# Kernel tuning notes

Hardware: AMD Instinct MI355X
Metric: run time of the kernel (lower is better)

## Reference

```python
import jax, jax.numpy as jnp
import numpy as np

N_NODES = 100000
N_EDGES = 1600000
D_IN = 128
HIDDEN = 64
N_CLASSES = 10
N_GRAPHS = 512


def setup_inputs() -> dict:
    key = jax.random.key(0)
    ks = jax.random.split(key, 9)
    x = jax.random.normal(ks[0], (N_NODES, D_IN), dtype=jnp.float32)
    edge_index = jax.random.randint(ks[1], (2, N_EDGES), 0, N_NODES, dtype=jnp.int32)
    batch = jnp.sort(jax.random.randint(ks[2], (N_NODES,), 0, N_GRAPHS, dtype=jnp.int32))
    # GCNConv: lin (no bias) + separate bias added after aggregation
    s1 = 1.0 / np.sqrt(D_IN)
    s2 = 1.0 / np.sqrt(HIDDEN)
    W1 = jax.random.uniform(ks[3], (D_IN, HIDDEN), jnp.float32, -s1, s1)
    b1 = jnp.zeros((HIDDEN,), jnp.float32)
    W2 = jax.random.uniform(ks[4], (HIDDEN, HIDDEN), jnp.float32, -s2, s2)
    b2 = jnp.zeros((HIDDEN,), jnp.float32)
    Wfc = jax.random.uniform(ks[5], (HIDDEN, N_CLASSES), jnp.float32, -s2, s2)
    bfc = jax.random.uniform(ks[6], (N_CLASSES,), jnp.float32, -s2, s2)
    return {"x": x, "edge_index": edge_index, "batch": batch,
            "W1": W1, "b1": b1, "W2": W2, "b2": b2, "Wfc": Wfc, "bfc": bfc}


def gcn_conv(x, src, dst, W, b, n_nodes):
    # symmetric normalization with added self-loops (PyG gcn_norm defaults)
    deg = jnp.zeros((n_nodes,), x.dtype).at[dst].add(1.0) + 1.0  # +1 self-loop
    dinv = jax.lax.rsqrt(deg)
    h = x @ W  # [N, out]
    coef = (dinv[src] * dinv[dst])[:, None]          # [E, 1]
    msg = h[src] * coef                               # [E, out]
    agg = jax.ops.segment_sum(msg, dst, num_segments=n_nodes)
    agg = agg + h * (dinv * dinv)[:, None]            # self-loop contribution
    return agg + b


def reference(x, edge_index, batch, W1, b1, W2, b2, Wfc, bfc):
    src, dst = edge_index[0], edge_index[1]
    n_nodes = x.shape[0]
    h = gcn_conv(x, src, dst, W1, b1, n_nodes)
    h = jax.nn.relu(h)
    # dropout skipped (inference, training=False)
    h = gcn_conv(h, src, dst, W2, b2, n_nodes)
    h = jax.nn.relu(h)
    # global mean pool over graphs
    sums = jax.ops.segment_sum(h, batch, num_segments=N_GRAPHS)
    cnts = jax.ops.segment_sum(jnp.ones((n_nodes,), h.dtype), batch, num_segments=N_GRAPHS)
    pooled = sums / jnp.maximum(cnts, 1.0)[:, None]   # [G, hidden]
    logits = pooled @ Wfc + bfc                        # [G, classes]
    return jax.nn.log_softmax(logits, axis=1)
```

## Files before the change

### kernel.cpp

```cpp
#include <hip/hip_runtime.h>
#include <cstdint>
#include <cstddef>

#define N_NODES   100000
#define N_EDGES   1600000
#define D_IN      128
#define HIDDEN    64
#define N_GRAPHS  512
#define N_CLASSES 10

#define NB   196
#define EB   1563
#define EB4  391
#define NBE  (NB * EB)
#define BCAP 12288
#define PSLOTS 8

typedef __attribute__((ext_vector_type(8))) short bf16x8;
typedef __attribute__((ext_vector_type(4))) float f32x4;
typedef __attribute__((ext_vector_type(2))) float f32x2;

__device__ inline float bf2f(unsigned short u) {
    return __uint_as_float(((unsigned int)u) << 16);
}
__device__ inline unsigned short f2bf(float f) {
    unsigned int x = __float_as_uint(f);
    return (unsigned short)((x + 0x7FFF + ((x >> 16) & 1)) >> 16);
}

__global__ __launch_bounds__(256)
void scan1_kernel(const int* __restrict__ in, int* __restrict__ bsum, int n) {
    __shared__ int lds[256];
    int tid = threadIdx.x;
    int base = blockIdx.x * 4096 + tid * 16;
    int s = 0;
#pragma unroll
    for (int j = 0; j < 16; j++) { int i = base + j; if (i < n) s += in[i]; }
    lds[tid] = s; __syncthreads();
    for (int off = 128; off > 0; off >>= 1) {
        if (tid < off) lds[tid] += lds[tid + off];
        __syncthreads();
    }
    if (tid == 0) bsum[blockIdx.x] = lds[0];
}

__global__ __launch_bounds__(256)
void scan2_kernel(int* __restrict__ bsum, int* __restrict__ out, int nb, int n) {
    __shared__ int lds[256];
    int tid = threadIdx.x;
    int v = (tid < nb) ? bsum[tid] : 0;
    lds[tid] = v; __syncthreads();
    for (int off = 1; off < 256; off <<= 1) {
        int t = (tid >= off) ? lds[tid - off] : 0;
        __syncthreads();
        lds[tid] += t;
        __syncthreads();
    }
    if (tid < nb) bsum[tid] = lds[tid] - v;
    if (tid == 255) out[n] = lds[255];
}

__global__ __launch_bounds__(256)
void scan3_kernel(const int* __restrict__ in, const int* __restrict__ bsum,
                  int* __restrict__ out, int n) {
    __shared__ int lds[256];
    int tid = threadIdx.x;
    int base = blockIdx.x * 4096 + tid * 16;
    int v[16]; int s = 0;
#pragma unroll
    for (int j = 0; j < 16; j++) {
        int i = base + j;
        v[j] = (i < n) ? in[i] : 0;
        s += v[j];
    }
    lds[tid] = s; __syncthreads();
    for (int off = 1; off < 256; off <<= 1) {
        int t = (tid >= off) ? lds[tid - off] : 0;
        __syncthreads();
        lds[tid] += t;
        __syncthreads();
    }
    int ex = lds[tid] - s + bsum[blockIdx.x];
#pragma unroll
    for (int j = 0; j < 16; j++) {
        int i = base + j;
        if (i < n) { out[i] = ex; ex += v[j]; }
    }
}

__global__ __launch_bounds__(256)
void hist_kernel(const int* __restrict__ dst, int* __restrict__ HA) {
    __shared__ int cnt[NB];
    const int tid = threadIdx.x;
    const int hb = blockIdx.x;
    for (int i = tid; i < NB; i += 256) cnt[i] = 0;
    __syncthreads();
    int base = hb * 1024 + tid;
#pragma unroll
    for (int j = 0; j < 4; j++) {
        int t = base + j * 256;
        if (t < N_EDGES) atomicAdd(&cnt[dst[t] >> 9], 1);
    }
    __syncthreads();
    for (int b = tid; b < NB; b += 256) HA[b * EB + hb] = cnt[b];
}

__global__ __launch_bounds__(256)
void scatterA2_kernel(const int* __restrict__ src, const int* __restrict__ dst,
                      const int* __restrict__ posA, unsigned int* __restrict__ edgeA) {
    __shared__ int off[NB];
    int tid = threadIdx.x, blk = blockIdx.x;
    for (int b = tid; b < NB; b += 256) off[b] = posA[b * EB + blk * 4];
    __syncthreads();
    int base = blk * 4096 + tid;
#pragma unroll
    for (int j = 0; j < 16; j++) {
        int t = base + j * 256;
        if (t < N_EDGES) {
            int d = dst[t];
            unsigned int pk = (((unsigned int)(d & 511)) << 17) | (unsigned int)src[t];
            int r = atomicAdd(&off[d >> 9], 1);
            edgeA[r] = pk;
        }
    }
}

__global__ __launch_bounds__(256)
void passB_kernel(const int* __restrict__ posA, const unsigned int* __restrict__ edgeA,
                  int* __restrict__ noffs, float* __restrict__ dinv,
                  int* __restrict__ srcs2) {
    __shared__ int hist[512];
    __shared__ int off[512];
    __shared__ int ps[256];
    __shared__ int srcs_l[BCAP];

    int tid = threadIdx.x, b = blockIdx.x;
    int e0 = posA[b * EB];
    int e1 = posA[(b + 1) * EB];
    int n0 = b << 9;
    int nn = min(512, N_NODES - n0);
    int len = e1 - e0;

    hist[tid] = 0; hist[tid + 256] = 0;
    __syncthreads();
    for (int i = e0 + tid; i < e1; i += 256) atomicAdd(&hist[edgeA[i] >> 17], 1);
    __syncthreads();

    for (int n = tid; n < nn; n += 256) dinv[n0 + n] = rsqrtf((float)hist[n] + 1.0f);

    int a0 = hist[2 * tid], a1 = hist[2 * tid + 1];
    ps[tid] = a0 + a1;
    __syncthreads();
    for (int d = 1; d < 256; d <<= 1) {
        int v = (tid >= d) ? ps[tid - d] : 0;
        __syncthreads();
        ps[tid] += v;
        __syncthreads();
    }
    int pre = ps[tid] - (a0 + a1);
    off[2 * tid] = pre;
    off[2 * tid + 1] = pre + a0;
    __syncthreads();

    for (int n = tid; n < nn; n += 256) noffs[n0 + n] = e0 + off[n];
    if (b == NB - 1 && tid == 0) noffs[N_NODES] = N_EDGES;
    __syncthreads();

    if (len <= BCAP) {
        for (int i = e0 + tid; i < e1; i += 256) {
            unsigned int e = edgeA[i];
            int r = atomicAdd(&off[e >> 17], 1);
            srcs_l[r] = (int)(e & 0x1FFFFu);
        }
        __syncthreads();
        for (int i = tid; i < len; i += 256) srcs2[e0 + i] = srcs_l[i];
    } else {
        for (int i = e0 + tid; i < e1; i += 256) {
            unsigned int e = edgeA[i];
            int r = atomicAdd(&off[e >> 17], 1);
            srcs2[e0 + r] = (int)(e & 0x1FFFFu);
        }
    }
}

__global__ __launch_bounds__(512)
void gemm1_kernel(const float* __restrict__ X, const float* __restrict__ W,
                  const float* __restrict__ dinv, unsigned short* __restrict__ H,
                  int n_rows) {
    constexpr int K  = D_IN;
    constexpr int KP = K + 8;
    __shared__ unsigned short Wt[64 * KP];

    const int tid  = threadIdx.x;
    const int row0 = blockIdx.x * 128;

    for (int i = tid; i < K * 64; i += 512) {
        int k = i >> 6;
        int n = i & 63;
        Wt[n * KP + k] = f2bf(W[i]);
    }

    const int wave = tid >> 6;
    const int lane = tid & 63;
    const int lrow = lane & 15;
    const int quad = lane >> 4;
    const int m = wave * 16 + lrow;
    const int row = row0 + m;
    const bool valid = row < n_rows;

    float4 xa[8];
    if (valid) {
        const float4* xr4 = (const float4*)(X + (size_t)row * K);
#pragma unroll
        for (int kt = 0; kt < 4; kt++) {
            int q = (kt * 32 + quad * 8) >> 2;
            xa[2 * kt]     = xr4[q];
            xa[2 * kt + 1] = xr4[q + 1];
        }
    } else {
#pragma unroll
        for (int j = 0; j < 8; j++) xa[j] = make_float4(0.f, 0.f, 0.f, 0.f);
    }
    __syncthreads();

    f32x4 acc0 = {0.f, 0.f, 0.f, 0.f};
    f32x4 acc1 = {0.f, 0.f, 0.f, 0.f};
    f32x4 acc2 = {0.f, 0.f, 0.f, 0.f};
    f32x4 acc3 = {0.f, 0.f, 0.f, 0.f};

#pragma unroll
    for (int kt = 0; kt < 4; kt++) {
        int k0 = kt * 32 + quad * 8;
        const float* f = (const float*)&xa[2 * kt];
        bf16x8 a;
#pragma unroll
        for (int j = 0; j < 8; j++) a[j] = (short)f2bf(f[j]);
        bf16x8 b0 = *(const bf16x8*)&Wt[(0 * 16 + lrow) * KP + k0];
        bf16x8 b1 = *(const bf16x8*)&Wt[(1 * 16 + lrow) * KP + k0];
        bf16x8 b2 = *(const bf16x8*)&Wt[(2 * 16 + lrow) * KP + k0];
        bf16x8 b3 = *(const bf16x8*)&Wt[(3 * 16 + lrow) * KP + k0];
        acc0 = __builtin_amdgcn_mfma_f32_16x16x32_bf16(a, b0, acc0, 0, 0, 0);
        acc1 = __builtin_amdgcn_mfma_f32_16x16x32_bf16(a, b1, acc1, 0, 0, 0);
        acc2 = __builtin_amdgcn_mfma_f32_16x16x32_bf16(a, b2, acc2, 0, 0, 0);
        acc3 = __builtin_amdgcn_mfma_f32_16x16x32_bf16(a, b3, acc3, 0, 0, 0);
    }

    f32x4 accs[4] = {acc0, acc1, acc2, acc3};
#pragma unroll
    for (int r = 0; r < 4; r++) {
        int orow = row0 + wave * 16 + quad * 4 + r;
        if (orow < n_rows) {
            float dv = dinv[orow];
#pragma unroll
            for (int c = 0; c < 4; c++)
                H[(size_t)orow * 64 + c * 16 + lrow] = f2bf(accs[c][r] * dv);
        }
    }
}

__device__ inline void upk_add(int4 u, float* acc) {
    unsigned int a = (unsigned int)u.x, b = (unsigned int)u.y;
    unsigned int d = (unsigned int)u.z, e = (unsigned int)u.w;
    acc[0] += __uint_as_float(a << 16);
    acc[1] += __uint_as_float(a & 0xFFFF0000u);
    acc[2] += __uint_as_float(b << 16);
    acc[3] += __uint_as_float(b & 0xFFFF0000u);
    acc[4] += __uint_as_float(d << 16);
    acc[5] += __uint_as_float(d & 0xFFFF0000u);
    acc[6] += __uint_as_float(e << 16);
    acc[7] += __uint_as_float(e & 0xFFFF0000u);
}

__device__ inline void upk8_add(int2 u, float* acc) {
    f32x2 p0 = __builtin_amdgcn_cvt_pk_f32_fp8(u.x, false);
    f32x2 p1 = __builtin_amdgcn_cvt_pk_f32_fp8(u.x, true);
    f32x2 p2 = __builtin_amdgcn_cvt_pk_f32_fp8(u.y, false);
    f32x2 p3 = __builtin_amdgcn_cvt_pk_f32_fp8(u.y, true);
    acc[0] += p0.x; acc[1] += p0.y;
    acc[2] += p1.x; acc[3] += p1.y;
    acc[4] += p2.x; acc[5] += p2.y;
    acc[6] += p3.x; acc[7] += p3.y;
}

__global__ __launch_bounds__(512)
void gather1_gemm2_kernel(const int* __restrict__ offs, const int* __restrict__ srcs,
                          const float* __restrict__ dinv, const unsigned short* __restrict__ h,
                          const float* __restrict__ b1v, const float* __restrict__ W2,
                          unsigned char* __restrict__ H8, int n_nodes) {
    constexpr int KP = 72;
    __shared__ unsigned short Hs[64 * KP];
    __shared__ unsigned short Wt[64 * KP];

    const int tid   = threadIdx.x;
    const int node0 = blockIdx.x * 64;

    for (int i = tid; i < 64 * 64; i += 512) {
        int k = i >> 6;
        int n = i & 63;
        Wt[n * KP + k] = f2bf(W2[i]);
    }

    const int g    = tid >> 3;
    const int node = node0 + g;
    const int cg   = (tid & 7) * 8;

    float acc[8];
#pragma unroll
    for (int j = 0; j < 8; j++) acc[j] = 0.f;
    float dn = 0.f;

    if (node < n_nodes) {
        dn = dinv[node];
        int4 us = *(const int4*)(h + (size_t)node * 64 + cg);
        upk_add(us, acc);

        int i = offs[node];
        const int i1 = offs[node + 1];
        int rem = i1 - i;
        if (rem > 0) {
            int s[8];
#pragma unroll
            for (int j = 0; j < 8; j++) s[j] = srcs[i + (j < rem ? j : rem - 1)];
            while (rem > 0) {
                int4 u8[8];
#pragma unroll
                for (int j = 0; j < 8; j++)
                    u8[j] = *(const int4*)(h + (size_t)s[j] * 64 + cg);
                const int cur  = rem < 8 ? rem : 8;
                const int ni   = i + cur;
                const int nrem = rem - cur;
                if (nrem > 0) {
#pragma unroll
                    for (int j = 0; j < 8; j++)
                        s[j] = srcs[ni + (j < nrem ? j : nrem - 1)];
                }
#pragma unroll
                for (int j = 0; j < 8; j++) { if (j < cur) upk_add(u8[j], acc); }
                i = ni; rem = nrem;
            }
        }
    }

    {
        float4 bv0 = *(const float4*)(b1v + cg);
        float4 bv1 = *(const float4*)(b1v + cg + 4);
        float r0 = fmaxf(dn * acc[0] + bv0.x, 0.f);
        float r1 = fmaxf(dn * acc[1] + bv0.y, 0.f);
        float r2 = fmaxf(dn * acc[2] + bv0.z, 0.f);
        float r3 = fmaxf(dn * acc[3] + bv0.w, 0.f);
        float r4 = fmaxf(dn * acc[4] + bv1.x, 0.f);
        float r5 = fmaxf(dn * acc[5] + bv1.y, 0.f);
        float r6 = fmaxf(dn * acc[6] + bv1.z, 0.f);
        float r7 = fmaxf(dn * acc[7] + bv1.w, 0.f);
        ushort4 p0 = make_ushort4(f2bf(r0), f2bf(r1), f2bf(r2), f2bf(r3));
        ushort4 p1 = make_ushort4(f2bf(r4), f2bf(r5), f2bf(r6), f2bf(r7));
        *(ushort4*)&Hs[g * KP + cg]     = p0;
        *(ushort4*)&Hs[g * KP + cg + 4] = p1;
    }
    __syncthreads();

    const int wave = tid >> 6;
    const int lane = tid & 63;
    const int lrow = lane & 15;
    const int quad = lane >> 4;
    const int rt = (wave & 3) * 16;
    const int ct = (wave >> 2) * 32;
    const int m = rt + lrow;

    f32x4 acc0 = {0.f, 0.f, 0.f, 0.f};
    f32x4 acc1 = {0.f, 0.f, 0.f, 0.f};
#pragma unroll
    for (int kt = 0; kt < 2; kt++) {
        int k0 = kt * 32 + quad * 8;
        bf16x8 a  = *(const bf16x8*)&Hs[m * KP + k0];
        bf16x8 w0 = *(const bf16x8*)&Wt[(ct + lrow) * KP + k0];
        bf16x8 w1 = *(const bf16x8*)&Wt[(ct + 16 + lrow) * KP + k0];
        acc0 = __builtin_amdgcn_mfma_f32_16x16x32_bf16(a, w0, acc0, 0, 0, 0);
        acc1 = __builtin_amdgcn_mfma_f32_16x16x32_bf16(a, w1, acc1, 0, 0, 0);
    }

    f32x4 accs[2] = {acc0, acc1};
#pragma unroll
    for (int r = 0; r < 4; r++) {
        int row = node0 + rt + quad * 4 + r;
        if (row < n_nodes) {
            float dv = dinv[row];
#pragma unroll
            for (int c = 0; c < 2; c++) {
                float v = accs[c][r] * dv;
                int p = __builtin_amdgcn_cvt_pk_fp8_f32(v, v, 0, false);
                H8[(size_t)row * 64 + ct + c * 16 + lrow] = (unsigned char)(p & 0xFF);
            }
        }
    }
}

__global__ __launch_bounds__(256)
void gather_fp8_pool_kernel(const int* __restrict__ offs, const int* __restrict__ srcs,
                            const float* __restrict__ dinv, const unsigned char* __restrict__ h8,
                            const float* __restrict__ b, const int* __restrict__ batch,
                            float* __restrict__ pooled, float* __restrict__ cnt,
                            int n_nodes) {
    __shared__ float pacc[PSLOTS][64];
    __shared__ float lcnt[PSLOTS];
    __shared__ int sg[2];

    int tid = threadIdx.x;
    int node0 = blockIdx.x * 32;
    int lastn = min(node0 + 31, n_nodes - 1);
    for (int i = tid; i < PSLOTS * 64; i += 256) ((float*)pacc)[i] = 0.f;
    if (tid < PSLOTS) lcnt[tid] = 0.f;
    if (tid == 0) { sg[0] = batch[min(node0, n_nodes - 1)]; sg[1] = batch[lastn]; }
    __syncthreads();
    int g0 = sg[0];
    bool single = (sg[0] == sg[1]);

    int node = node0 + (tid >> 3);
    int cg = (tid & 7) * 8;

    float r[8];
#pragma unroll
    for (int j = 0; j < 8; j++) r[j] = 0.f;

    if (node < n_nodes) {
        float dn = dinv[node];
        float acc[8];
#pragma unroll
        for (int j = 0; j < 8; j++) acc[j] = 0.f;
        {
            int2 u = *(const int2*)(h8 + (size_t)node * 64 + cg);
            upk8_add(u, acc);
        }

        int i = offs[node];
        const int i1 = offs[node + 1];
        int rem = i1 - i;
        if (rem > 0) {
            int s[8];
#pragma unroll
            for (int j = 0; j < 8; j++) s[j] = srcs[i + (j < rem ? j : rem - 1)];
            while (rem > 0) {
                int2 u8[8];
#pragma unroll
                for (int j = 0; j < 8; j++)
                    u8[j] = *(const int2*)(h8 + (size_t)s[j] * 64 + cg);
                const int cur  = rem < 8 ? rem : 8;
                const int ni   = i + cur;
                const int nrem = rem - cur;
                if (nrem > 0) {
#pragma unroll
                    for (int j = 0; j < 8; j++)
                        s[j] = srcs[ni + (j < nrem ? j : nrem - 1)];
                }
#pragma unroll
                for (int j = 0; j < 8; j++) { if (j < cur) upk8_add(u8[j], acc); }
                i = ni; rem = nrem;
            }
        }

        float4 b0 = *(const float4*)(b + cg);
        float4 b1 = *(const float4*)(b + cg + 4);
        r[0] = fmaxf(dn * acc[0] + b0.x, 0.f);
        r[1] = fmaxf(dn * acc[1] + b0.y, 0.f);
        r[2] = fmaxf(dn * acc[2] + b0.z, 0.f);
        r[3] = fmaxf(dn * acc[3] + b0.w, 0.f);
        r[4] = fmaxf(dn * acc[4] + b1.x, 0.f);
        r[5] = fmaxf(dn * acc[5] + b1.y, 0.f);
        r[6] = fmaxf(dn * acc[6] + b1.z, 0.f);
        r[7] = fmaxf(dn * acc[7] + b1.w, 0.f);
    }

    if (single) {
#pragma unroll
        for (int j = 0; j < 8; j++) {
            float v = r[j];
            v += __shfl_xor(v, 8);
            v += __shfl_xor(v, 16);
            v += __shfl_xor(v, 32);
            r[j] = v;
        }
        int wave = tid >> 6;
        int lane = tid & 63;
        if (lane < 8) {
#pragma unroll
            for (int j = 0; j < 8; j++) pacc[wave][lane * 8 + j] = r[j];
        }
        __syncthreads();
        if (tid < 64) {
            float s = pacc[0][tid] + pacc[1][tid] + pacc[2][tid] + pacc[3][tid];
            if (s != 0.f) unsafeAtomicAdd(&pooled[(size_t)g0 * 64 + tid], s);
        }
        if (tid == 0) {
            int valid = min(32, n_nodes - node0);
            unsafeAtomicAdd(&cnt[g0], (float)valid);
        }
    } else {
        if (node < n_nodes) {
            int g = batch[node];
            int slot = g - g0;
            if (slot < PSLOTS) {
#pragma unroll
                for (int j = 0; j < 8; j++) atomicAdd(&pacc[slot][cg + j], r[j]);
                if ((tid & 7) == 0) atomicAdd(&lcnt[slot], 1.f);
            } else {
#pragma unroll
                for (int j = 0; j < 8; j++) unsafeAtomicAdd(&pooled[(size_t)g * 64 + cg + j], r[j]);
                if ((tid & 7) == 0) unsafeAtomicAdd(&cnt[g], 1.f);
            }
        }
        __syncthreads();
        for (int i = tid; i < PSLOTS * 64; i += 256) {
            float v = ((float*)pacc)[i];
            if (v != 0.f) unsafeAtomicAdd(&pooled[(size_t)(g0 + (i >> 6)) * 64 + (i & 63)], v);
        }
        if (tid < PSLOTS && lcnt[tid] != 0.f) unsafeAtomicAdd(&cnt[g0 + tid], lcnt[tid]);
    }
}

__global__ __launch_bounds__(256)
void head_kernel(const float* __restrict__ pooled, const float* __restrict__ cnt,
                 const float* __restrict__ Wfc, const float* __restrict__ bfc,
                 float* __restrict__ out) {
    __shared__ float Ws[HIDDEN * N_CLASSES];
    __shared__ float bs[N_CLASSES];
    int tid = threadIdx.x;
    for (int i = tid; i < HIDDEN * N_CLASSES; i += 256) Ws[i] = Wfc[i];
    if (tid < N_CLASSES) bs[tid] = bfc[tid];
    __syncthreads();

    int g = blockIdx.x * 256 + tid;
    if (g >= N_GRAPHS) return;

    float inv = 1.f / fmaxf(cnt[g], 1.f);
    float p[HIDDEN];
#pragma unroll
    for (int k = 0; k < HIDDEN; k++) p[k] = pooled[(size_t)g * 64 + k] * inv;

    float lg[N_CLASSES];
    float m = -1e30f;
#pragma unroll
    for (int j = 0; j < N_CLASSES; j++) {
        float a = bs[j];
#pragma unroll
        for (int k = 0; k < HIDDEN; k++) a += p[k] * Ws[k * N_CLASSES + j];
        lg[j] = a;
        m = fmaxf(m, a);
    }
    float s = 0.f;
#pragma unroll
    for (int j = 0; j < N_CLASSES; j++) s += __expf(lg[j] - m);
    float lse = m + __logf(s);
#pragma unroll
    for (int j = 0; j < N_CLASSES; j++) out[(size_t)g * N_CLASSES + j] = lg[j] - lse;
}

extern "C" void kernel_launch(void* const* d_in, const int* in_sizes, int n_in,
                              void* d_out, int out_size, void* d_ws, size_t ws_size,
                              hipStream_t stream) {
    const float* x   = (const float*)d_in[0];
    const int*   ei  = (const int*)d_in[1];
    const int*   bat = (const int*)d_in[2];
    const float* W1  = (const float*)d_in[3];
    const float* b1  = (const float*)d_in[4];
    const float* W2  = (const float*)d_in[5];
    const float* b2  = (const float*)d_in[6];
    const float* Wfc = (const float*)d_in[7];
    const float* bfc = (const float*)d_in[8];
    float* out = (float*)d_out;

    const int* src = ei;
    const int* dst = ei + N_EDGES;

    char* ws = (char*)d_ws;

    const size_t OFF_H     = 0;
    const size_t OFF_SRCS2 = 12800000;
    const size_t OFF_NOFFS = 19200000;
    const size_t OFF_DINV  = 19600016;
    const size_t OFF_BUFB  = 25600000;
    const size_t OFF_EDGEA = 38400000;
    const size_t OFF_HA    = 51200000;
    const size_t OFF_POSA  = 52425392;
    const size_t OFF_BSUM  = 53650800;
    const size_t OFF_POOL  = 53651824;
    const size_t OFF_CNT   = 53782896;

    unsigned short* hbuf  = (unsigned short*)(ws + OFF_H);
    int*   srcs2  = (int*)  (ws + OFF_SRCS2);
    int*   noffs  = (int*)  (ws + OFF_NOFFS);
    float* dinv   = (float*)(ws + OFF_DINV);
    unsigned char* hbuf8 = (unsigned char*)(ws + OFF_BUFB);
    unsigned int* edgeA = (unsigned int*)(ws + OFF_EDGEA);
    int*   HA     = (int*)  (ws + OFF_HA);
    int*   posA   = (int*)  (ws + OFF_POSA);
    int*   bsum   = (int*)  (ws + OFF_BSUM);
    float* pooled = (float*)(ws + OFF_POOL);
    float* cnt    = (float*)(ws + OFF_CNT);

    const int SCAN_BLOCKS = (NBE + 4095) / 4096;
    const int GATHER_BLOCKS = (N_NODES * 8 + 255) / 256;
    const int GEMM2_BLOCKS = (N_NODES + 63) / 64;
    const int GEMM1_BLOCKS = (N_NODES + 127) / 128;

    hipMemsetAsync(pooled, 0, (size_t)(N_GRAPHS * 64 + N_GRAPHS) * sizeof(float), stream);

    hist_kernel<<<EB, 256, 0, stream>>>(dst, HA);
    scan1_kernel<<<SCAN_BLOCKS, 256, 0, stream>>>(HA, bsum, NBE);
    scan2_kernel<<<1, 256, 0, stream>>>(bsum, posA, SCAN_BLOCKS, NBE);
    scan3_kernel<<<SCAN_BLOCKS, 256, 0, stream>>>(HA, bsum, posA, NBE);
    scatterA2_kernel<<<EB4, 256, 0, stream>>>(src, dst, posA, edgeA);
    passB_kernel<<<NB, 256, 0, stream>>>(posA, edgeA, noffs, dinv, srcs2);
    gemm1_kernel<<<GEMM1_BLOCKS, 512, 0, stream>>>(x, W1, dinv, hbuf, N_NODES);
    gather1_gemm2_kernel<<<GEMM2_BLOCKS, 512, 0, stream>>>(
        noffs, srcs2, dinv, hbuf, b1, W2, hbuf8, N_NODES);
    gather_fp8_pool_kernel<<<GATHER_BLOCKS, 256, 0, stream>>>(
        noffs, srcs2, dinv, hbuf8, b2, bat, pooled, cnt, N_NODES);

    head_kernel<<<(N_GRAPHS + 255) / 256, 256, 0, stream>>>(pooled, cnt, Wfc, bfc, out);
}
```

Before: 230.3 us.

## Replace per-block histogram scan with atomic bucket totals and LDS-staged scatter

The CSR build changes. A large per-block histogram and its three-kernel prefix scan give way to global atomic bucket totals, a single 196-entry scan, and a scatter that claims bucket ranges with atomics and stages edges in LDS. passB now caches the bucket's edges in LDS so it avoids a second global read. Both gather loops prefetch 16 neighbours instead of 8 to raise memory-level parallelism. The costs are nondeterministic edge order within buckets, more LDS in passB (which may lower occupancy), and more registers in the gathers.

```diff
diff --git a/kernel.cpp b/kernel.cpp
--- a/kernel.cpp
+++ b/kernel.cpp
@@ -10,9 +10,7 @@
 #define N_CLASSES 10
 
 #define NB   196
-#define EB   1563
 #define EB4  391
-#define NBE  (NB * EB)
 #define BCAP 12288
 #define PSLOTS 8
 
@@ -29,26 +27,30 @@
 }
 
 __global__ __launch_bounds__(256)
-void scan1_kernel(const int* __restrict__ in, int* __restrict__ bsum, int n) {
+void hist2_kernel(const int* __restrict__ dst, int* __restrict__ bucketTot) {
+    __shared__ int cnt[NB];
+    const int tid = threadIdx.x;
+    for (int i = tid; i < NB; i += 256) cnt[i] = 0;
+    __syncthreads();
+    int base = blockIdx.x * 4096 + tid;
+#pragma unroll
+    for (int j = 0; j < 16; j++) {
+        int t = base + j * 256;
+        if (t < N_EDGES) atomicAdd(&cnt[dst[t] >> 9], 1);
+    }
+    __syncthreads();
+    for (int b = tid; b < NB; b += 256) {
+        int c = cnt[b];
+        if (c) atomicAdd(&bucketTot[b], c);
+    }
+}
+
+__global__ __launch_bounds__(256)
+void scan196_kernel(const int* __restrict__ bucketTot, int* __restrict__ bucketBase,
+                    int* __restrict__ bucketCur) {
     __shared__ int lds[256];
     int tid = threadIdx.x;
-    int base = blockIdx.x * 4096 + tid * 16;
-    int s = 0;
-#pragma unroll
-    for (int j = 0; j < 16; j++) { int i = base + j; if (i < n) s += in[i]; }
-    lds[tid] = s; __syncthreads();
-    for (int off = 128; off > 0; off >>= 1) {
-        if (tid < off) lds[tid] += lds[tid + off];
-        __syncthreads();
-    }
-    if (tid == 0) bsum[blockIdx.x] = lds[0];
-}
-
-__global__ __launch_bounds__(256)
-void scan2_kernel(int* __restrict__ bsum, int* __restrict__ out, int nb, int n) {
-    __shared__ int lds[256];
-    int tid = threadIdx.x;
-    int v = (tid < nb) ? bsum[tid] : 0;
+    int v = (tid < NB) ? bucketTot[tid] : 0;
     lds[tid] = v; __syncthreads();
     for (int off = 1; off < 256; off <<= 1) {
         int t = (tid >= off) ? lds[tid - off] : 0;
@@ -56,94 +58,75 @@
         lds[tid] += t;
         __syncthreads();
     }
-    if (tid < nb) bsum[tid] = lds[tid] - v;
-    if (tid == 255) out[n] = lds[255];
+    int ex = lds[tid] - v;
+    if (tid < NB) { bucketBase[tid] = ex; bucketCur[tid] = ex; }
+    if (tid == 255) bucketBase[NB] = lds[255];
 }
 
 __global__ __launch_bounds__(256)
-void scan3_kernel(const int* __restrict__ in, const int* __restrict__ bsum,
-                  int* __restrict__ out, int n) {
-    __shared__ int lds[256];
-    int tid = threadIdx.x;
-    int base = blockIdx.x * 4096 + tid * 16;
-    int v[16]; int s = 0;
-#pragma unroll
-    for (int j = 0; j < 16; j++) {
-        int i = base + j;
-        v[j] = (i < n) ? in[i] : 0;
-        s += v[j];
-    }
-    lds[tid] = s; __syncthreads();
-    for (int off = 1; off < 256; off <<= 1) {
-        int t = (tid >= off) ? lds[tid - off] : 0;
-        __syncthreads();
-        lds[tid] += t;
-        __syncthreads();
-    }
-    int ex = lds[tid] - s + bsum[blockIdx.x];
-#pragma unroll
-    for (int j = 0; j < 16; j++) {
-        int i = base + j;
-        if (i < n) { out[i] = ex; ex += v[j]; }
-    }
-}
-
-__global__ __launch_bounds__(256)
-void hist_kernel(const int* __restrict__ dst, int* __restrict__ HA) {
+void scatter_kernel(const int* __restrict__ src, const int* __restrict__ dst,
+                    int* __restrict__ bucketCur, unsigned int* __restrict__ edgeA) {
+    __shared__ unsigned int epk[4096];
+    __shared__ unsigned char ebk[4096];
     __shared__ int cnt[NB];
-    const int tid = threadIdx.x;
-    const int hb = blockIdx.x;
-    for (int i = tid; i < NB; i += 256) cnt[i] = 0;
-    __syncthreads();
-    int base = hb * 1024 + tid;
-#pragma unroll
-    for (int j = 0; j < 4; j++) {
-        int t = base + j * 256;
-        if (t < N_EDGES) atomicAdd(&cnt[dst[t] >> 9], 1);
-    }
-    __syncthreads();
-    for (int b = tid; b < NB; b += 256) HA[b * EB + hb] = cnt[b];
-}
-
-__global__ __launch_bounds__(256)
-void scatterA2_kernel(const int* __restrict__ src, const int* __restrict__ dst,
-                      const int* __restrict__ posA, unsigned int* __restrict__ edgeA) {
     __shared__ int off[NB];
     int tid = threadIdx.x, blk = blockIdx.x;
-    for (int b = tid; b < NB; b += 256) off[b] = posA[b * EB + blk * 4];
-    __syncthreads();
-    int base = blk * 4096 + tid;
+    for (int i = tid; i < NB; i += 256) cnt[i] = 0;
+    __syncthreads();
+    int base = blk * 4096;
 #pragma unroll
     for (int j = 0; j < 16; j++) {
-        int t = base + j * 256;
+        int li = j * 256 + tid;
+        int t = base + li;
         if (t < N_EDGES) {
             int d = dst[t];
-            unsigned int pk = (((unsigned int)(d & 511)) << 17) | (unsigned int)src[t];
-            int r = atomicAdd(&off[d >> 9], 1);
-            edgeA[r] = pk;
-        }
+            epk[li] = (((unsigned int)(d & 511)) << 17) | (unsigned int)src[t];
+            ebk[li] = (unsigned char)(d >> 9);
+            atomicAdd(&cnt[d >> 9], 1);
+        }
+    }
+    __syncthreads();
+    for (int b = tid; b < NB; b += 256) {
+        int c = cnt[b];
+        off[b] = c ? atomicAdd(&bucketCur[b], c) : 0;
+    }
+    __syncthreads();
+    int nmax = min(4096, N_EDGES - base);
+    for (int li = tid; li < nmax; li += 256) {
+        int b = ebk[li];
+        int r = atomicAdd(&off[b], 1);
+        edgeA[r] = epk[li];
     }
 }
 
 __global__ __launch_bounds__(256)
-void passB_kernel(const int* __restrict__ posA, const unsigned int* __restrict__ edgeA,
+void passB_kernel(const int* __restrict__ bucketBase, const unsigned int* __restrict__ edgeA,
                   int* __restrict__ noffs, float* __restrict__ dinv,
                   int* __restrict__ srcs2) {
     __shared__ int hist[512];
     __shared__ int off[512];
     __shared__ int ps[256];
+    __shared__ unsigned int eds[BCAP];
     __shared__ int srcs_l[BCAP];
 
     int tid = threadIdx.x, b = blockIdx.x;
-    int e0 = posA[b * EB];
-    int e1 = posA[(b + 1) * EB];
+    int e0 = bucketBase[b];
+    int e1 = bucketBase[b + 1];
     int n0 = b << 9;
     int nn = min(512, N_NODES - n0);
     int len = e1 - e0;
 
     hist[tid] = 0; hist[tid + 256] = 0;
     __syncthreads();
-    for (int i = e0 + tid; i < e1; i += 256) atomicAdd(&hist[edgeA[i] >> 17], 1);
+    if (len <= BCAP) {
+        for (int i = tid; i < len; i += 256) {
+            unsigned int e = edgeA[e0 + i];
+            eds[i] = e;
+            atomicAdd(&hist[e >> 17], 1);
+        }
+    } else {
+        for (int i = tid; i < len; i += 256) atomicAdd(&hist[edgeA[e0 + i] >> 17], 1);
+    }
     __syncthreads();
 
     for (int n = tid; n < nn; n += 256) dinv[n0 + n] = rsqrtf((float)hist[n] + 1.0f);
@@ -167,16 +150,16 @@
     __syncthreads();
 
     if (len <= BCAP) {
-        for (int i = e0 + tid; i < e1; i += 256) {
-            unsigned int e = edgeA[i];
+        for (int i = tid; i < len; i += 256) {
+            unsigned int e = eds[i];
             int r = atomicAdd(&off[e >> 17], 1);
             srcs_l[r] = (int)(e & 0x1FFFFu);
         }
         __syncthreads();
         for (int i = tid; i < len; i += 256) srcs2[e0 + i] = srcs_l[i];
     } else {
-        for (int i = e0 + tid; i < e1; i += 256) {
-            unsigned int e = edgeA[i];
+        for (int i = tid; i < len; i += 256) {
+            unsigned int e = edgeA[e0 + i];
             int r = atomicAdd(&off[e >> 17], 1);
             srcs2[e0 + r] = (int)(e & 0x1FFFFu);
         }
@@ -318,24 +301,24 @@
         const int i1 = offs[node + 1];
         int rem = i1 - i;
         if (rem > 0) {
-            int s[8];
-#pragma unroll
-            for (int j = 0; j < 8; j++) s[j] = srcs[i + (j < rem ? j : rem - 1)];
+            int s[16];
+#pragma unroll
+            for (int j = 0; j < 16; j++) s[j] = srcs[i + (j < rem ? j : rem - 1)];
             while (rem > 0) {
-                int4 u8[8];
-#pragma unroll
-                for (int j = 0; j < 8; j++)
-                    u8[j] = *(const int4*)(h + (size_t)s[j] * 64 + cg);
-                const int cur  = rem < 8 ? rem : 8;
+                int4 u16[16];
+#pragma unroll
+                for (int j = 0; j < 16; j++)
+                    u16[j] = *(const int4*)(h + (size_t)s[j] * 64 + cg);
+                const int cur  = rem < 16 ? rem : 16;
                 const int ni   = i + cur;
                 const int nrem = rem - cur;
                 if (nrem > 0) {
 #pragma unroll
-                    for (int j = 0; j < 8; j++)
+                    for (int j = 0; j < 16; j++)
                         s[j] = srcs[ni + (j < nrem ? j : nrem - 1)];
                 }
 #pragma unroll
-                for (int j = 0; j < 8; j++) { if (j < cur) upk_add(u8[j], acc); }
+                for (int j = 0; j < 16; j++) { if (j < cur) upk_add(u16[j], acc); }
                 i = ni; rem = nrem;
             }
         }
@@ -436,24 +419,24 @@
         const int i1 = offs[node + 1];
         int rem = i1 - i;
         if (rem > 0) {
-            int s[8];
-#pragma unroll
-            for (int j = 0; j < 8; j++) s[j] = srcs[i + (j < rem ? j : rem - 1)];
+            int s[16];
+#pragma unroll
+            for (int j = 0; j < 16; j++) s[j] = srcs[i + (j < rem ? j : rem - 1)];
             while (rem > 0) {
-                int2 u8[8];
-#pragma unroll
-                for (int j = 0; j < 8; j++)
-                    u8[j] = *(const int2*)(h8 + (size_t)s[j] * 64 + cg);
-                const int cur  = rem < 8 ? rem : 8;
+                int2 u16[16];
+#pragma unroll
+                for (int j = 0; j < 16; j++)
+                    u16[j] = *(const int2*)(h8 + (size_t)s[j] * 64 + cg);
+                const int cur  = rem < 16 ? rem : 16;
                 const int ni   = i + cur;
                 const int nrem = rem - cur;
                 if (nrem > 0) {
 #pragma unroll
-                    for (int j = 0; j < 8; j++)
+                    for (int j = 0; j < 16; j++)
                         s[j] = srcs[ni + (j < nrem ? j : nrem - 1)];
                 }
 #pragma unroll
-                for (int j = 0; j < 8; j++) { if (j < cur) upk8_add(u8[j], acc); }
+                for (int j = 0; j < 16; j++) { if (j < cur) upk8_add(u16[j], acc); }
                 i = ni; rem = nrem;
             }
         }
@@ -579,11 +562,11 @@
     const size_t OFF_DINV  = 19600016;
     const size_t OFF_BUFB  = 25600000;
     const size_t OFF_EDGEA = 38400000;
-    const size_t OFF_HA    = 51200000;
-    const size_t OFF_POSA  = 52425392;
-    const size_t OFF_BSUM  = 53650800;
-    const size_t OFF_POOL  = 53651824;
-    const size_t OFF_CNT   = 53782896;
+    const size_t OFF_POOL  = 44800000;
+    const size_t OFF_CNT   = 44931072;
+    const size_t OFF_BTOT  = 44933120;
+    const size_t OFF_BBASE = 44933904;
+    const size_t OFF_BCUR  = 44934692;
 
     unsigned short* hbuf  = (unsigned short*)(ws + OFF_H);
     int*   srcs2  = (int*)  (ws + OFF_SRCS2);
@@ -591,25 +574,22 @@
     float* dinv   = (float*)(ws + OFF_DINV);
     unsigned char* hbuf8 = (unsigned char*)(ws + OFF_BUFB);
     unsigned int* edgeA = (unsigned int*)(ws + OFF_EDGEA);
-    int*   HA     = (int*)  (ws + OFF_HA);
-    int*   posA   = (int*)  (ws + OFF_POSA);
-    int*   bsum   = (int*)  (ws + OFF_BSUM);
     float* pooled = (float*)(ws + OFF_POOL);
     float* cnt    = (float*)(ws + OFF_CNT);
-
-    const int SCAN_BLOCKS = (NBE + 4095) / 4096;
+    int* bucketTot  = (int*)(ws + OFF_BTOT);
+    int* bucketBase = (int*)(ws + OFF_BBASE);
+    int* bucketCur  = (int*)(ws + OFF_BCUR);
+
     const int GATHER_BLOCKS = (N_NODES * 8 + 255) / 256;
     const int GEMM2_BLOCKS = (N_NODES + 63) / 64;
     const int GEMM1_BLOCKS = (N_NODES + 127) / 128;
 
-    hipMemsetAsync(pooled, 0, (size_t)(N_GRAPHS * 64 + N_GRAPHS) * sizeof(float), stream);
-
-    hist_kernel<<<EB, 256, 0, stream>>>(dst, HA);
-    scan1_kernel<<<SCAN_BLOCKS, 256, 0, stream>>>(HA, bsum, NBE);
-    scan2_kernel<<<1, 256, 0, stream>>>(bsum, posA, SCAN_BLOCKS, NBE);
-    scan3_kernel<<<SCAN_BLOCKS, 256, 0, stream>>>(HA, bsum, posA, NBE);
-    scatterA2_kernel<<<EB4, 256, 0, stream>>>(src, dst, posA, edgeA);
-    passB_kernel<<<NB, 256, 0, stream>>>(posA, edgeA, noffs, dinv, srcs2);
+    hipMemsetAsync(pooled, 0, (size_t)(131072 + 2048 + 784), stream);
+
+    hist2_kernel<<<EB4, 256, 0, stream>>>(dst, bucketTot);
+    scan196_kernel<<<1, 256, 0, stream>>>(bucketTot, bucketBase, bucketCur);
+    scatter_kernel<<<EB4, 256, 0, stream>>>(src, dst, bucketCur, edgeA);
+    passB_kernel<<<NB, 256, 0, stream>>>(bucketBase, edgeA, noffs, dinv, srcs2);
     gemm1_kernel<<<GEMM1_BLOCKS, 512, 0, stream>>>(x, W1, dinv, hbuf, N_NODES);
     gather1_gemm2_kernel<<<GEMM2_BLOCKS, 512, 0, stream>>>(
         noffs, srcs2, dinv, hbuf, b1, W2, hbuf8, N_NODES);
```

Measured after the change: 257.2 us. 1.12x slower.

## Replace two-pass bucketed CSR build with global-atomic degree count and direct scatter

Applied to the files above, without the earlier changes.

Drops the coarse-bucket histogram, the bucket scatter and the per-bucket LDS sort used to build the CSR. Instead it counts per-node degrees with global atomics, scans the 100k degrees (also writing dinv and a cursor array), and scatters each edge source straight to its final slot with a global atomic on the destination's cursor. This removes several passes and the intermediate edgeA buffer, but adds heavy global atomic traffic and leaves neighbour order inside each node nondeterministic, which can slightly change float summation results. It also double-buffers the fp8 gather loop so the next 8 neighbour loads are issued before the current 8 are accumulated.

```diff
diff --git a/kernel.cpp b/kernel.cpp
--- a/kernel.cpp
+++ b/kernel.cpp
@@ -9,11 +9,8 @@
 #define N_GRAPHS  512
 #define N_CLASSES 10
 
-#define NB   196
-#define EB   1563
 #define EB4  391
-#define NBE  (NB * EB)
-#define BCAP 12288
+#define SCAN_BLOCKS 25
 #define PSLOTS 8
 
 typedef __attribute__((ext_vector_type(8))) short bf16x8;
@@ -26,6 +23,16 @@
 __device__ inline unsigned short f2bf(float f) {
     unsigned int x = __float_as_uint(f);
     return (unsigned short)((x + 0x7FFF + ((x >> 16) & 1)) >> 16);
+}
+
+__global__ __launch_bounds__(256)
+void degcnt_kernel(const int* __restrict__ dst, int* __restrict__ deg) {
+    int base = blockIdx.x * 4096 + threadIdx.x;
+#pragma unroll
+    for (int j = 0; j < 16; j++) {
+        int t = base + j * 256;
+        if (t < N_EDGES) atomicAdd(&deg[dst[t]], 1);
+    }
 }
 
 __global__ __launch_bounds__(256)
@@ -61,8 +68,9 @@
 }
 
 __global__ __launch_bounds__(256)
-void scan3_kernel(const int* __restrict__ in, const int* __restrict__ bsum,
-                  int* __restrict__ out, int n) {
+void scan3x_kernel(const int* __restrict__ deg, const int* __restrict__ bsum,
+                   int* __restrict__ noffs, int* __restrict__ nodeCur,
+                   float* __restrict__ dinv, int n) {
     __shared__ int lds[256];
     int tid = threadIdx.x;
     int base = blockIdx.x * 4096 + tid * 16;
@@ -70,7 +78,7 @@
 #pragma unroll
     for (int j = 0; j < 16; j++) {
         int i = base + j;
-        v[j] = (i < n) ? in[i] : 0;
+        v[j] = (i < n) ? deg[i] : 0;
         s += v[j];
     }
     lds[tid] = s; __syncthreads();
@@ -84,101 +92,26 @@
 #pragma unroll
     for (int j = 0; j < 16; j++) {
         int i = base + j;
-        if (i < n) { out[i] = ex; ex += v[j]; }
-    }
-}
-
-__global__ __launch_bounds__(256)
-void hist_kernel(const int* __restrict__ dst, int* __restrict__ HA) {
-    __shared__ int cnt[NB];
-    const int tid = threadIdx.x;
-    const int hb = blockIdx.x;
-    for (int i = tid; i < NB; i += 256) cnt[i] = 0;
-    __syncthreads();
-    int base = hb * 1024 + tid;
-#pragma unroll
-    for (int j = 0; j < 4; j++) {
-        int t = base + j * 256;
-        if (t < N_EDGES) atomicAdd(&cnt[dst[t] >> 9], 1);
-    }
-    __syncthreads();
-    for (int b = tid; b < NB; b += 256) HA[b * EB + hb] = cnt[b];
-}
-
-__global__ __launch_bounds__(256)
-void scatterA2_kernel(const int* __restrict__ src, const int* __restrict__ dst,
-                      const int* __restrict__ posA, unsigned int* __restrict__ edgeA) {
-    __shared__ int off[NB];
-    int tid = threadIdx.x, blk = blockIdx.x;
-    for (int b = tid; b < NB; b += 256) off[b] = posA[b * EB + blk * 4];
-    __syncthreads();
-    int base = blk * 4096 + tid;
+        if (i < n) {
+            noffs[i] = ex;
+            nodeCur[i] = ex;
+            dinv[i] = rsqrtf((float)v[j] + 1.0f);
+            ex += v[j];
+        }
+    }
+}
+
+__global__ __launch_bounds__(256)
+void scatter_direct_kernel(const int* __restrict__ src, const int* __restrict__ dst,
+                           int* __restrict__ nodeCur, int* __restrict__ srcs2) {
+    int base = blockIdx.x * 4096 + threadIdx.x;
 #pragma unroll
     for (int j = 0; j < 16; j++) {
         int t = base + j * 256;
         if (t < N_EDGES) {
             int d = dst[t];
-            unsigned int pk = (((unsigned int)(d & 511)) << 17) | (unsigned int)src[t];
-            int r = atomicAdd(&off[d >> 9], 1);
-            edgeA[r] = pk;
-        }
-    }
-}
-
-__global__ __launch_bounds__(256)
-void passB_kernel(const int* __restrict__ posA, const unsigned int* __restrict__ edgeA,
-                  int* __restrict__ noffs, float* __restrict__ dinv,
-                  int* __restrict__ srcs2) {
-    __shared__ int hist[512];
-    __shared__ int off[512];
-    __shared__ int ps[256];
-    __shared__ int srcs_l[BCAP];
-
-    int tid = threadIdx.x, b = blockIdx.x;
-    int e0 = posA[b * EB];
-    int e1 = posA[(b + 1) * EB];
-    int n0 = b << 9;
-    int nn = min(512, N_NODES - n0);
-    int len = e1 - e0;
-
-    hist[tid] = 0; hist[tid + 256] = 0;
-    __syncthreads();
-    for (int i = e0 + tid; i < e1; i += 256) atomicAdd(&hist[edgeA[i] >> 17], 1);
-    __syncthreads();
-
-    for (int n = tid; n < nn; n += 256) dinv[n0 + n] = rsqrtf((float)hist[n] + 1.0f);
-
-    int a0 = hist[2 * tid], a1 = hist[2 * tid + 1];
-    ps[tid] = a0 + a1;
-    __syncthreads();
-    for (int d = 1; d < 256; d <<= 1) {
-        int v = (tid >= d) ? ps[tid - d] : 0;
-        __syncthreads();
-        ps[tid] += v;
-        __syncthreads();
-    }
-    int pre = ps[tid] - (a0 + a1);
-    off[2 * tid] = pre;
-    off[2 * tid + 1] = pre + a0;
-    __syncthreads();
-
-    for (int n = tid; n < nn; n += 256) noffs[n0 + n] = e0 + off[n];
-    if (b == NB - 1 && tid == 0) noffs[N_NODES] = N_EDGES;
-    __syncthreads();
-
-    if (len <= BCAP) {
-        for (int i = e0 + tid; i < e1; i += 256) {
-            unsigned int e = edgeA[i];
-            int r = atomicAdd(&off[e >> 17], 1);
-            srcs_l[r] = (int)(e & 0x1FFFFu);
-        }
-        __syncthreads();
-        for (int i = tid; i < len; i += 256) srcs2[e0 + i] = srcs_l[i];
-    } else {
-        for (int i = e0 + tid; i < e1; i += 256) {
-            unsigned int e = edgeA[i];
-            int r = atomicAdd(&off[e >> 17], 1);
-            srcs2[e0 + r] = (int)(e & 0x1FFFFu);
+            int r = atomicAdd(&nodeCur[d], 1);
+            srcs2[r] = src[t];
         }
     }
 }
@@ -435,27 +368,37 @@
         int i = offs[node];
         const int i1 = offs[node + 1];
         int rem = i1 - i;
+
+        int curA = 0;
+        int2 uA[8];
         if (rem > 0) {
-            int s[8];
-#pragma unroll
-            for (int j = 0; j < 8; j++) s[j] = srcs[i + (j < rem ? j : rem - 1)];
-            while (rem > 0) {
-                int2 u8[8];
+            curA = rem < 8 ? rem : 8;
+            int sA[8];
+#pragma unroll
+            for (int j = 0; j < 8; j++) sA[j] = srcs[i + (j < curA ? j : curA - 1)];
+#pragma unroll
+            for (int j = 0; j < 8; j++)
+                uA[j] = *(const int2*)(h8 + (size_t)sA[j] * 64 + cg);
+            i += curA; rem -= curA;
+        }
+        while (curA > 0) {
+            int curB = 0;
+            int2 uB[8];
+            if (rem > 0) {
+                curB = rem < 8 ? rem : 8;
+                int sB[8];
+#pragma unroll
+                for (int j = 0; j < 8; j++) sB[j] = srcs[i + (j < curB ? j : curB - 1)];
 #pragma unroll
                 for (int j = 0; j < 8; j++)
-                    u8[j] = *(const int2*)(h8 + (size_t)s[j] * 64 + cg);
-                const int cur  = rem < 8 ? rem : 8;
-                const int ni   = i + cur;
-                const int nrem = rem - cur;
-                if (nrem > 0) {
-#pragma unroll
-                    for (int j = 0; j < 8; j++)
-                        s[j] = srcs[ni + (j < nrem ? j : nrem - 1)];
-                }
-#pragma unroll
-                for (int j = 0; j < 8; j++) { if (j < cur) upk8_add(u8[j], acc); }
-                i = ni; rem = nrem;
+                    uB[j] = *(const int2*)(h8 + (size_t)sB[j] * 64 + cg);
+                i += curB; rem -= curB;
             }
+#pragma unroll
+            for (int j = 0; j < 8; j++) { if (j < curA) upk8_add(uA[j], acc); }
+#pragma unroll
+            for (int j = 0; j < 8; j++) uA[j] = uB[j];
+            curA = curB;
         }
 
         float4 b0 = *(const float4*)(b + cg);
@@ -578,38 +521,34 @@
     const size_t OFF_NOFFS = 19200000;
     const size_t OFF_DINV  = 19600016;
     const size_t OFF_BUFB  = 25600000;
-    const size_t OFF_EDGEA = 38400000;
-    const size_t OFF_HA    = 51200000;
-    const size_t OFF_POSA  = 52425392;
-    const size_t OFF_BSUM  = 53650800;
-    const size_t OFF_POOL  = 53651824;
-    const size_t OFF_CNT   = 53782896;
+    const size_t OFF_DEG   = 32000000;
+    const size_t OFF_POOL  = 32400000;
+    const size_t OFF_CNT   = 32531072;
+    const size_t OFF_NCUR  = 32533120;
+    const size_t OFF_BSUM  = 32933120;
 
     unsigned short* hbuf  = (unsigned short*)(ws + OFF_H);
     int*   srcs2  = (int*)  (ws + OFF_SRCS2);
     int*   noffs  = (int*)  (ws + OFF_NOFFS);
     float* dinv   = (float*)(ws + OFF_DINV);
     unsigned char* hbuf8 = (unsigned char*)(ws + OFF_BUFB);
-    unsigned int* edgeA = (unsigned int*)(ws + OFF_EDGEA);
-    int*   HA     = (int*)  (ws + OFF_HA);
-    int*   posA   = (int*)  (ws + OFF_POSA);
-    int*   bsum   = (int*)  (ws + OFF_BSUM);
+    int*   deg    = (int*)  (ws + OFF_DEG);
     float* pooled = (float*)(ws + OFF_POOL);
     float* cnt    = (float*)(ws + OFF_CNT);
-
-    const int SCAN_BLOCKS = (NBE + 4095) / 4096;
+    int*   nodeCur = (int*) (ws + OFF_NCUR);
+    int*   bsum   = (int*)  (ws + OFF_BSUM);
+
     const int GATHER_BLOCKS = (N_NODES * 8 + 255) / 256;
     const int GEMM2_BLOCKS = (N_NODES + 63) / 64;
     const int GEMM1_BLOCKS = (N_NODES + 127) / 128;
 
-    hipMemsetAsync(pooled, 0, (size_t)(N_GRAPHS * 64 + N_GRAPHS) * sizeof(float), stream);
-
-    hist_kernel<<<EB, 256, 0, stream>>>(dst, HA);
-    scan1_kernel<<<SCAN_BLOCKS, 256, 0, stream>>>(HA, bsum, NBE);
-    scan2_kernel<<<1, 256, 0, stream>>>(bsum, posA, SCAN_BLOCKS, NBE);
-    scan3_kernel<<<SCAN_BLOCKS, 256, 0, stream>>>(HA, bsum, posA, NBE);
-    scatterA2_kernel<<<EB4, 256, 0, stream>>>(src, dst, posA, edgeA);
-    passB_kernel<<<NB, 256, 0, stream>>>(posA, edgeA, noffs, dinv, srcs2);
+    hipMemsetAsync(deg, 0, (size_t)(400000 + 131072 + 2048), stream);
+
+    degcnt_kernel<<<EB4, 256, 0, stream>>>(dst, deg);
+    scan1_kernel<<<SCAN_BLOCKS, 256, 0, stream>>>(deg, bsum, N_NODES);
+    scan2_kernel<<<1, 256, 0, stream>>>(bsum, noffs, SCAN_BLOCKS, N_NODES);
+    scan3x_kernel<<<SCAN_BLOCKS, 256, 0, stream>>>(deg, bsum, noffs, nodeCur, dinv, N_NODES);
+    scatter_direct_kernel<<<EB4, 256, 0, stream>>>(src, dst, nodeCur, srcs2);
     gemm1_kernel<<<GEMM1_BLOCKS, 512, 0, stream>>>(x, W1, dinv, hbuf, N_NODES);
     gather1_gemm2_kernel<<<GEMM2_BLOCKS, 512, 0, stream>>>(
         noffs, srcs2, dinv, hbuf, b1, W2, hbuf8, N_NODES);
```

After: 393.0 us. +70.6%, slower.

## Sort nodes by degree for layer-1 gather and fuse scan passes

Applied to the files above, without the earlier changes.

Adds a degree histogram in passB, a 64-bin scan, and a permutation scatter. gather1_gemm2 then processes nodes in degree-sorted order, which should balance per-wave gather loop lengths. Merges the single-block scan2 into scan3 so each block rescans the block sums itself, removing one launch. It adds two small kernels plus an extra memset and indirect row indexing, which scatters the output writes and costs locality. The write of noffs[N_NODES] is also dropped.

```diff
diff --git a/kernel.cpp b/kernel.cpp
--- a/kernel.cpp
+++ b/kernel.cpp
@@ -15,6 +15,7 @@
 #define NBE  (NB * EB)
 #define BCAP 12288
 #define PSLOTS 8
+#define PBLK 25
 
 typedef __attribute__((ext_vector_type(8))) short bf16x8;
 typedef __attribute__((ext_vector_type(4))) float f32x4;
@@ -45,26 +46,23 @@
 }
 
 __global__ __launch_bounds__(256)
-void scan2_kernel(int* __restrict__ bsum, int* __restrict__ out, int nb, int n) {
+void scan3b_kernel(const int* __restrict__ in, const int* __restrict__ bsum,
+                   int* __restrict__ out, int n, int nb) {
+    __shared__ int bscan[256];
     __shared__ int lds[256];
     int tid = threadIdx.x;
-    int v = (tid < nb) ? bsum[tid] : 0;
-    lds[tid] = v; __syncthreads();
+    int bv = (tid < nb) ? bsum[tid] : 0;
+    bscan[tid] = bv; __syncthreads();
     for (int off = 1; off < 256; off <<= 1) {
-        int t = (tid >= off) ? lds[tid - off] : 0;
-        __syncthreads();
-        lds[tid] += t;
-        __syncthreads();
-    }
-    if (tid < nb) bsum[tid] = lds[tid] - v;
-    if (tid == 255) out[n] = lds[255];
-}
-
-__global__ __launch_bounds__(256)
-void scan3_kernel(const int* __restrict__ in, const int* __restrict__ bsum,
-                  int* __restrict__ out, int n) {
-    __shared__ int lds[256];
-    int tid = threadIdx.x;
+        int t = (tid >= off) ? bscan[tid - off] : 0;
+        __syncthreads();
+        bscan[tid] += t;
+        __syncthreads();
+    }
+    bscan[tid] -= bv;
+    __syncthreads();
+    int blockoff = bscan[blockIdx.x];
+
     int base = blockIdx.x * 4096 + tid * 16;
     int v[16]; int s = 0;
 #pragma unroll
@@ -80,12 +78,13 @@
         lds[tid] += t;
         __syncthreads();
     }
-    int ex = lds[tid] - s + bsum[blockIdx.x];
+    int ex = lds[tid] - s + blockoff;
 #pragma unroll
     for (int j = 0; j < 16; j++) {
         int i = base + j;
         if (i < n) { out[i] = ex; ex += v[j]; }
     }
+    if (blockIdx.x == 0 && tid == 0) out[n] = N_EDGES;
 }
 
 __global__ __launch_bounds__(256)
@@ -128,10 +127,12 @@
 __global__ __launch_bounds__(256)
 void passB_kernel(const int* __restrict__ posA, const unsigned int* __restrict__ edgeA,
                   int* __restrict__ noffs, float* __restrict__ dinv,
-                  int* __restrict__ srcs2) {
+                  int* __restrict__ srcs2, unsigned char* __restrict__ deg8,
+                  int* __restrict__ dbin) {
     __shared__ int hist[512];
     __shared__ int off[512];
     __shared__ int ps[256];
+    __shared__ int dbin_l[64];
     __shared__ int srcs_l[BCAP];
 
     int tid = threadIdx.x, b = blockIdx.x;
@@ -142,11 +143,18 @@
     int len = e1 - e0;
 
     hist[tid] = 0; hist[tid + 256] = 0;
+    if (tid < 64) dbin_l[tid] = 0;
     __syncthreads();
     for (int i = e0 + tid; i < e1; i += 256) atomicAdd(&hist[edgeA[i] >> 17], 1);
     __syncthreads();
 
-    for (int n = tid; n < nn; n += 256) dinv[n0 + n] = rsqrtf((float)hist[n] + 1.0f);
+    for (int n = tid; n < nn; n += 256) {
+        int d = hist[n];
+        dinv[n0 + n] = rsqrtf((float)d + 1.0f);
+        int bin = min(d, 63);
+        deg8[n0 + n] = (unsigned char)bin;
+        atomicAdd(&dbin_l[bin], 1);
+    }
 
     int a0 = hist[2 * tid], a1 = hist[2 * tid + 1];
     ps[tid] = a0 + a1;
@@ -163,7 +171,7 @@
     __syncthreads();
 
     for (int n = tid; n < nn; n += 256) noffs[n0 + n] = e0 + off[n];
-    if (b == NB - 1 && tid == 0) noffs[N_NODES] = N_EDGES;
+    if (tid < 64) { int c = dbin_l[tid]; if (c) atomicAdd(&dbin[tid], c); }
     __syncthreads();
 
     if (len <= BCAP) {
@@ -179,6 +187,48 @@
             unsigned int e = edgeA[i];
             int r = atomicAdd(&off[e >> 17], 1);
             srcs2[e0 + r] = (int)(e & 0x1FFFFu);
+        }
+    }
+}
+
+__global__ __launch_bounds__(64)
+void scan64_kernel(const int* __restrict__ dbin, int* __restrict__ binCur) {
+    int tid = threadIdx.x;
+    int v = dbin[tid];
+    int s = v;
+    for (int off = 1; off < 64; off <<= 1) {
+        int t = __shfl_up(s, off);
+        if (tid >= off) s += t;
+    }
+    binCur[tid] = s - v;
+}
+
+__global__ __launch_bounds__(256)
+void permscatter_kernel(const unsigned char* __restrict__ deg8, int* __restrict__ binCur,
+                        int* __restrict__ perm, int n) {
+    __shared__ int cnt[64];
+    __shared__ int off[64];
+    __shared__ unsigned char db[4096];
+    int tid = threadIdx.x;
+    if (tid < 64) cnt[tid] = 0;
+    __syncthreads();
+    int base = blockIdx.x * 4096;
+#pragma unroll
+    for (int j = 0; j < 16; j++) {
+        int i = base + j * 256 + tid;
+        unsigned char d = (i < n) ? deg8[i] : 255;
+        db[j * 256 + tid] = d;
+        if (i < n) atomicAdd(&cnt[d], 1);
+    }
+    __syncthreads();
+    if (tid < 64) { int c = cnt[tid]; off[tid] = c ? atomicAdd(&binCur[tid], c) : 0; }
+    __syncthreads();
+#pragma unroll
+    for (int j = 0; j < 16; j++) {
+        int i = base + j * 256 + tid;
+        if (i < n) {
+            int r = atomicAdd(&off[db[j * 256 + tid]], 1);
+            perm[r] = i;
         }
     }
 }
@@ -286,6 +336,7 @@
 void gather1_gemm2_kernel(const int* __restrict__ offs, const int* __restrict__ srcs,
                           const float* __restrict__ dinv, const unsigned short* __restrict__ h,
                           const float* __restrict__ b1v, const float* __restrict__ W2,
+                          const int* __restrict__ perm,
                           unsigned char* __restrict__ H8, int n_nodes) {
     constexpr int KP = 72;
     __shared__ unsigned short Hs[64 * KP];
@@ -301,7 +352,7 @@
     }
 
     const int g    = tid >> 3;
-    const int node = node0 + g;
+    const int pidx = node0 + g;
     const int cg   = (tid & 7) * 8;
 
     float acc[8];
@@ -309,7 +360,8 @@
     for (int j = 0; j < 8; j++) acc[j] = 0.f;
     float dn = 0.f;
 
-    if (node < n_nodes) {
+    if (pidx < n_nodes) {
+        const int node = perm[pidx];
         dn = dinv[node];
         int4 us = *(const int4*)(h + (size_t)node * 64 + cg);
         upk_add(us, acc);
@@ -382,14 +434,15 @@
     f32x4 accs[2] = {acc0, acc1};
 #pragma unroll
     for (int r = 0; r < 4; r++) {
-        int row = node0 + rt + quad * 4 + r;
-        if (row < n_nodes) {
-            float dv = dinv[row];
+        int rowi = node0 + rt + quad * 4 + r;
+        if (rowi < n_nodes) {
+            int prow = perm[rowi];
+            float dv = dinv[prow];
 #pragma unroll
             for (int c = 0; c < 2; c++) {
                 float v = accs[c][r] * dv;
                 int p = __builtin_amdgcn_cvt_pk_fp8_f32(v, v, 0, false);
-                H8[(size_t)row * 64 + ct + c * 16 + lrow] = (unsigned char)(p & 0xFF);
+                H8[(size_t)prow * 64 + ct + c * 16 + lrow] = (unsigned char)(p & 0xFF);
             }
         }
     }
@@ -579,6 +632,10 @@
     const size_t OFF_DINV  = 19600016;
     const size_t OFF_BUFB  = 25600000;
     const size_t OFF_EDGEA = 38400000;
+    const size_t OFF_PERM  = 44800000;
+    const size_t OFF_DEG8  = 45200000;
+    const size_t OFF_DBIN  = 45300096;
+    const size_t OFF_BCUR  = 45300352;
     const size_t OFF_HA    = 51200000;
     const size_t OFF_POSA  = 52425392;
     const size_t OFF_BSUM  = 53650800;
@@ -591,6 +648,10 @@
     float* dinv   = (float*)(ws + OFF_DINV);
     unsigned char* hbuf8 = (unsigned char*)(ws + OFF_BUFB);
     unsigned int* edgeA = (unsigned int*)(ws + OFF_EDGEA);
+    int*   perm   = (int*)  (ws + OFF_PERM);
+    unsigned char* deg8 = (unsigned char*)(ws + OFF_DEG8);
+    int*   dbin   = (int*)  (ws + OFF_DBIN);
+    int*   binCur = (int*)  (ws + OFF_BCUR);
     int*   HA     = (int*)  (ws + OFF_HA);
     int*   posA   = (int*)  (ws + OFF_POSA);
     int*   bsum   = (int*)  (ws + OFF_BSUM);
@@ -602,17 +663,19 @@
     const int GEMM2_BLOCKS = (N_NODES + 63) / 64;
     const int GEMM1_BLOCKS = (N_NODES + 127) / 128;
 
-    hipMemsetAsync(pooled, 0, (size_t)(N_GRAPHS * 64 + N_GRAPHS) * sizeof(float), stream);
+    hipMemsetAsync(pooled, 0, (size_t)(131072 + 2048), stream);
+    hipMemsetAsync(dbin, 0, 256, stream);
 
     hist_kernel<<<EB, 256, 0, stream>>>(dst, HA);
     scan1_kernel<<<SCAN_BLOCKS, 256, 0, stream>>>(HA, bsum, NBE);
-    scan2_kernel<<<1, 256, 0, stream>>>(bsum, posA, SCAN_BLOCKS, NBE);
-    scan3_kernel<<<SCAN_BLOCKS, 256, 0, stream>>>(HA, bsum, posA, NBE);
+    scan3b_kernel<<<SCAN_BLOCKS, 256, 0, stream>>>(HA, bsum, posA, NBE, SCAN_BLOCKS);
     scatterA2_kernel<<<EB4, 256, 0, stream>>>(src, dst, posA, edgeA);
-    passB_kernel<<<NB, 256, 0, stream>>>(posA, edgeA, noffs, dinv, srcs2);
+    passB_kernel<<<NB, 256, 0, stream>>>(posA, edgeA, noffs, dinv, srcs2, deg8, dbin);
+    scan64_kernel<<<1, 64, 0, stream>>>(dbin, binCur);
+    permscatter_kernel<<<PBLK, 256, 0, stream>>>(deg8, binCur, perm, N_NODES);
     gemm1_kernel<<<GEMM1_BLOCKS, 512, 0, stream>>>(x, W1, dinv, hbuf, N_NODES);
     gather1_gemm2_kernel<<<GEMM2_BLOCKS, 512, 0, stream>>>(
-        noffs, srcs2, dinv, hbuf, b1, W2, hbuf8, N_NODES);
+        noffs, srcs2, dinv, hbuf, b1, W2, perm, hbuf8, N_NODES);
     gather_fp8_pool_kernel<<<GATHER_BLOCKS, 256, 0, stream>>>(
         noffs, srcs2, dinv, hbuf8, b2, bat, pooled, cnt, N_NODES);
 
```

Result: slower. 246.7 us (+7.1%).
